# Kernel optimization log

Hardware: AMD Instinct MI355X
Metric: run time of the kernel (lower is better)

The kernel has to match this reference:

```python
import jax, jax.numpy as jnp
import numpy as np

B, S, H, E, I = 2, 2048, 1024, 8, 4096
NUM_SELECT = 2


def setup_inputs() -> dict:
    key = jax.random.key(0)
    ks = jax.random.split(key, 6)
    scale = 0.02
    x = jax.random.normal(ks[0], (B, S, H), dtype=jnp.float32)
    Wg = jax.random.normal(ks[1], (H, E), dtype=jnp.float32) * scale
    W1 = jax.random.normal(ks[2], (E, H, I), dtype=jnp.float32) * scale
    b1 = jnp.zeros((E, I), dtype=jnp.float32)
    W2 = jax.random.normal(ks[3], (E, I, H), dtype=jnp.float32) * scale
    b2 = jnp.zeros((E, H), dtype=jnp.float32)
    return {"x": x, "Wg": Wg, "W1": W1, "b1": b1, "W2": W2, "b2": b2}


def reference(x, Wg, W1, b1, W2, b2):
    b, s, h = x.shape
    e = Wg.shape[1]
    xf = x.reshape(-1, h)                       # [T, H], T = b*s
    T = xf.shape[0]

    logits = xf @ Wg                            # [T, E]
    probs = jax.nn.softmax(logits, axis=-1)
    topk_p, topk_i = jax.lax.top_k(probs, NUM_SELECT)   # [T, k]
    topk_p = topk_p / topk_p.sum(axis=-1, keepdims=True)

    # combine weight per (token, expert): w[t, e] = sum_k topk_p[t, k] * 1[topk_i[t, k] == e]
    # top_k indices within a row are distinct, so scatter-add is exact.
    w = jnp.zeros((T, e), dtype=xf.dtype).at[jnp.arange(T)[:, None], topk_i].add(topk_p)

    # Dense per-expert FFN, weighted combine (weight is 0 for unrouted tokens,
    # so math matches the masked gather/scatter loop of the original).
    out = jnp.zeros_like(xf)
    for ei in range(e):  # small fixed loop over experts
        hdn = jax.nn.silu(xf @ W1[ei] + b1[ei])          # [T, I]
        y = hdn @ W2[ei] + b2[ei]                        # [T, H]
        out = out + w[:, ei:ei + 1] * y
    return out.reshape(b, s, h)
```

## Files before the change

kernel.cpp:

```cpp
#include <hip/hip_runtime.h>
#include <cstdint>
#include <cstddef>

using u16 = unsigned short;
typedef __bf16 bf16x8 __attribute__((ext_vector_type(8)));
typedef float f32x4 __attribute__((ext_vector_type(4)));

#define T_TOK 4096
#define HDIM 1024
#define EXP 8
#define IDIM 4096
#define NROWS 8192
#define PAD_ROWS 8448
#define BM 256
#define MAX_TILES 40

__device__ __forceinline__ u16 f2bf(float f) {
  union { float f; uint32_t u; } v; v.f = f;
  uint32_t u = v.u;
  u += 0x7fffu + ((u >> 16) & 1u);
  return (u16)(u >> 16);
}

__device__ __forceinline__ void async_copy16(const u16* g, u16* s) {
  __builtin_amdgcn_global_load_lds((__attribute__((address_space(1))) void*)(void*)g,
                                   (__attribute__((address_space(3))) void*)s, 16, 0, 0);
}

__global__ __launch_bounds__(256) void gate_kernel(const float* __restrict__ x,
                                                   const float* __restrict__ Wg,
                                                   int* __restrict__ sel_e,
                                                   float* __restrict__ sel_w) {
  int lane = threadIdx.x & 63;
  int wave = threadIdx.x >> 6;
  int t = blockIdx.x * 4 + wave;
  const float* xr = x + (size_t)t * HDIM;
  float p[8];
#pragma unroll
  for (int e = 0; e < 8; ++e) p[e] = 0.f;
#pragma unroll
  for (int i = 0; i < 16; ++i) {
    int h = i * 64 + lane;
    float xv = xr[h];
    const float4* w4 = (const float4*)(Wg + h * 8);
    float4 a = w4[0], b = w4[1];
    p[0] += xv * a.x; p[1] += xv * a.y; p[2] += xv * a.z; p[3] += xv * a.w;
    p[4] += xv * b.x; p[5] += xv * b.y; p[6] += xv * b.z; p[7] += xv * b.w;
  }
#pragma unroll
  for (int e = 0; e < 8; ++e) {
#pragma unroll
    for (int off = 32; off > 0; off >>= 1) p[e] += __shfl_xor(p[e], off);
  }
  if (lane == 0) {
    int e0 = 0; float m0 = p[0];
#pragma unroll
    for (int e = 1; e < 8; ++e) { if (p[e] > m0) { m0 = p[e]; e0 = e; } }
    int e1 = -1; float m1 = -3.4e38f;
#pragma unroll
    for (int e = 0; e < 8; ++e) { if (e != e0 && p[e] > m1) { m1 = p[e]; e1 = e; } }
    float r = expf(m1 - m0);
    float w0 = 1.f / (1.f + r);
    float w1 = r / (1.f + r);
    sel_e[2 * t] = e0; sel_e[2 * t + 1] = e1;
    sel_w[2 * t] = w0; sel_w[2 * t + 1] = w1;
  }
}

__global__ void route_kernel(const int* __restrict__ sel_e, const float* __restrict__ sel_w,
                             int* __restrict__ row_token, float* __restrict__ row_weight,
                             int* __restrict__ tile_m0, int* __restrict__ tile_nrows,
                             int* __restrict__ tile_start, int* __restrict__ tile_cnt,
                             int* __restrict__ work_ctr) {
  __shared__ int cnt[EXP], off[EXP], cur[EXP];
  int tid = threadIdx.x;
  if (tid < EXP) { cnt[tid] = 0; cur[tid] = 0; }
  if (tid < 16) work_ctr[tid] = 0;
  __syncthreads();
  for (int i = tid; i < NROWS; i += 256) atomicAdd(&cnt[sel_e[i]], 1);
  __syncthreads();
  if (tid == 0) {
    int running = 0, nt = 0;
    for (int e = 0; e < EXP; ++e) {
      off[e] = running;
      int c = cnt[e];
      int ntile = (c + BM - 1) / BM;
      tile_start[e] = nt;
      tile_cnt[e] = ntile;
      for (int j = 0; j < ntile; ++j) {
        tile_m0[nt] = running + j * BM;
        tile_nrows[nt] = min(BM, c - j * BM);
        ++nt;
      }
      running += c;
    }
  }
  __syncthreads();
  for (int i = tid; i < NROWS; i += 256) {
    int e = sel_e[i];
    int pos = off[e] + atomicAdd(&cur[e], 1);
    row_token[pos] = i >> 1;
    row_weight[pos] = sel_w[i];
  }
}

__global__ __launch_bounds__(256) void gather_kernel(const float* __restrict__ x,
                                                     const int* __restrict__ row_token,
                                                     u16* __restrict__ xg) {
  int r = blockIdx.x;
  int tok = row_token[r];
  const float4* xs = (const float4*)(x + (size_t)tok * HDIM);
  float4 v = xs[threadIdx.x];
  ushort4 o;
  o.x = f2bf(v.x); o.y = f2bf(v.y); o.z = f2bf(v.z); o.w = f2bf(v.w);
  *(ushort4*)(xg + (size_t)r * HDIM + threadIdx.x * 4) = o;
}

__global__ __launch_bounds__(256) void transpose_convert(const float* __restrict__ src,
                                                         u16* __restrict__ dst, int R, int C) {
  int eb = blockIdx.z;
  const float* s = src + (size_t)eb * R * C;
  u16* d = dst + (size_t)eb * R * C;
  int cb = blockIdx.x * 64, rb = blockIdx.y * 64;
  __shared__ u16 tile[64][65];
  int tid = threadIdx.x;
#pragma unroll
  for (int i = 0; i < 4; ++i) {
    int idx = i * 256 + tid;
    int r = idx >> 4;
    int cq = (idx & 15) * 4;
    float4 v = *(const float4*)(s + (size_t)(rb + r) * C + cb + cq);
    tile[r][cq]     = f2bf(v.x);
    tile[r][cq + 1] = f2bf(v.y);
    tile[r][cq + 2] = f2bf(v.z);
    tile[r][cq + 3] = f2bf(v.w);
  }
  __syncthreads();
#pragma unroll
  for (int i = 0; i < 4; ++i) {
    int idx = i * 256 + tid;
    int c = idx >> 4;
    int rq = (idx & 15) * 4;
    ushort4 o;
    o.x = tile[rq][c]; o.y = tile[rq + 1][c]; o.z = tile[rq + 2][c]; o.w = tile[rq + 3][c];
    *(ushort4*)(d + (size_t)(cb + c) * R + rb + rq) = o;
  }
}

template <int K, int KS, int NB, bool SECOND>
__global__ __launch_bounds__(512, 2) void ffn_gemm8(
    const u16* __restrict__ A, const u16* __restrict__ B,
    const float* __restrict__ bias, u16* __restrict__ hdn_out,
    float* __restrict__ out, const int* __restrict__ row_token,
    const float* __restrict__ row_weight, const int* __restrict__ tile_m0,
    const int* __restrict__ tile_nrows, const int* __restrict__ tile_start,
    const int* __restrict__ tile_cnt, int* __restrict__ ctr, int N) {
  constexpr int KT = K / KS / 64;

  __shared__ u16 sA[2][2 * 128 * 64];
  __shared__ u16 sB[2][128 * 64];
  __shared__ int s_item;

  int tid = threadIdx.x;
  int lane = tid & 63;
  int wave = tid >> 6;
  int wm = wave >> 2, wn = wave & 3;
  int l15 = lane & 15, quad = lane >> 4;
  int r7 = l15 & 7;
  int xcd = blockIdx.x & 7;

  int c0 = tid, c1 = tid + 512;
  int r0s = c0 >> 3, j0 = ((c0 & 7) ^ (r0s & 7)) * 8;
  int r1s = c1 >> 3, j1 = ((c1 & 7) ^ (r1s & 7)) * 8;

  int jxk[2];
#pragma unroll
  for (int ks = 0; ks < 2; ++ks) jxk[ks] = ((ks * 4 + quad) ^ r7) * 8;

  for (int pass = 0; pass < 8; ++pass) {
    int ex = (xcd + pass) & 7;
    int nt_e = tile_cnt[ex];
    if (nt_e == 0) continue;
    int items = nt_e * NB * KS;
    int ts = tile_start[ex];

    for (;;) {
      if (tid == 0) s_item = atomicAdd(&ctr[ex], 1);
      __syncthreads();
      int its = s_item;
      if (its >= items) break;

      int per = NB * nt_e;
      int ksp = its / per;
      int rem = its - ksp * per;
      int nb = rem / nt_e;
      int tile = ts + (rem - nb * nt_e);

      int row0 = tile_m0[tile];
      int nrows = tile_nrows[tile];
      int n0 = nb * 128;
      int korg = ksp * (K / KS);

      const u16* Ab = A + (size_t)row0 * K + korg;
      const u16* Bb = B + (size_t)ex * (size_t)N * K + (size_t)n0 * K + korg;

      auto stageA = [&](int db, int sk, int ha) {
        async_copy16(Ab + (size_t)(ha * 128 + r0s) * K + sk * 64 + j0,
                     &sA[db][ha * 8192 + c0 * 8]);
        async_copy16(Ab + (size_t)(ha * 128 + r1s) * K + sk * 64 + j1,
                     &sA[db][ha * 8192 + c1 * 8]);
      };
      auto stageB = [&](int db, int sk) {
        async_copy16(Bb + (size_t)r0s * K + sk * 64 + j0, &sB[db][c0 * 8]);
        async_copy16(Bb + (size_t)r1s * K + sk * 64 + j1, &sB[db][c1 * 8]);
      };

      f32x4 acc[8][2];
#pragma unroll
      for (int am = 0; am < 8; ++am)
#pragma unroll
        for (int an = 0; an < 2; ++an) acc[am][an] = (f32x4){0.f, 0.f, 0.f, 0.f};

      stageA(0, 0, 0); stageA(0, 0, 1);
      stageB(0, 0);
      stageB(1, 1);
      asm volatile("s_waitcnt vmcnt(2)" ::: "memory");
      __builtin_amdgcn_s_barrier();

      for (int kt = 0; kt < KT; ++kt) {
        int cb = kt & 1, pb = cb ^ 1;
        int ka = kt + 1 < KT ? kt + 1 : KT - 1;
        int kb = kt + 2 < KT ? kt + 2 : KT - 1;
        const u16* sAc = sA[cb];
        const u16* sBc = sB[cb];

        bf16x8 bfr[2][2];
#pragma unroll
        for (int ks = 0; ks < 2; ++ks)
#pragma unroll
          for (int an = 0; an < 2; ++an)
            bfr[an][ks] = *(const bf16x8*)(sBc + ((wn * 2 + an) * 16 + l15) * 64 + jxk[ks]);

        {
          bf16x8 af[4][2];
#pragma unroll
          for (int ks = 0; ks < 2; ++ks)
#pragma unroll
            for (int i = 0; i < 4; ++i)
              af[i][ks] = *(const bf16x8*)(sAc + (wm * 128 + i * 16 + l15) * 64 + jxk[ks]);
          stageA(pb, ka, 0);
          stageA(pb, ka, 1);
          __builtin_amdgcn_s_barrier();
          __builtin_amdgcn_s_setprio(1);
#pragma unroll
          for (int i = 0; i < 4; ++i)
#pragma unroll
            for (int an = 0; an < 2; ++an)
#pragma unroll
              for (int ks = 0; ks < 2; ++ks)
                acc[i][an] = __builtin_amdgcn_mfma_f32_16x16x32_bf16(af[i][ks], bfr[an][ks],
                                                                    acc[i][an], 0, 0, 0);
          __builtin_amdgcn_s_setprio(0);
          __builtin_amdgcn_s_barrier();
        }
        {
          bf16x8 af[4][2];
#pragma unroll
          for (int ks = 0; ks < 2; ++ks)
#pragma unroll
            for (int i = 0; i < 4; ++i)
              af[i][ks] = *(const bf16x8*)(sAc + (wm * 128 + (4 + i) * 16 + l15) * 64 + jxk[ks]);
          stageB(cb, kb);
          asm volatile("s_waitcnt vmcnt(2)" ::: "memory");
          __builtin_amdgcn_s_barrier();
          __builtin_amdgcn_s_setprio(1);
#pragma unroll
          for (int i = 0; i < 4; ++i)
#pragma unroll
            for (int an = 0; an < 2; ++an)
#pragma unroll
              for (int ks = 0; ks < 2; ++ks)
                acc[4 + i][an] = __builtin_amdgcn_mfma_f32_16x16x32_bf16(af[i][ks], bfr[an][ks],
                                                                        acc[4 + i][an], 0, 0, 0);
          __builtin_amdgcn_s_setprio(0);
          __builtin_amdgcn_s_barrier();
        }
      }
      asm volatile("s_waitcnt vmcnt(0)" ::: "memory");

      if constexpr (!SECOND) {
#pragma unroll
        for (int an = 0; an < 2; ++an) {
          int col = n0 + (wn * 2 + an) * 16 + l15;
          float bv = bias[ex * N + col];
#pragma unroll
          for (int am = 0; am < 8; ++am) {
#pragma unroll
            for (int r = 0; r < 4; ++r) {
              int lr = wm * 128 + am * 16 + quad * 4 + r;
              if (lr < nrows) {
                float vv = acc[am][an][r] + bv;
                vv = vv / (1.f + __expf(-vv));
                hdn_out[(size_t)(row0 + lr) * N + col] = f2bf(vv);
              }
            }
          }
        }
      } else {
        float bv[2];
#pragma unroll
        for (int an = 0; an < 2; ++an)
          bv[an] = (ksp == 0) ? bias[ex * N + n0 + (wn * 2 + an) * 16 + l15] : 0.f;
#pragma unroll
        for (int am = 0; am < 8; ++am) {
#pragma unroll
          for (int r = 0; r < 4; ++r) {
            int lr = wm * 128 + am * 16 + quad * 4 + r;
            if (lr < nrows) {
              int grow = row0 + lr;
              int tok = row_token[grow];
              float w = row_weight[grow];
              float* orow = out + (size_t)tok * N;
#pragma unroll
              for (int an = 0; an < 2; ++an) {
                int col = n0 + (wn * 2 + an) * 16 + l15;
                atomicAdd(orow + col, (acc[am][an][r] + bv[an]) * w);
              }
            }
          }
        }
      }
    }
  }
}

extern "C" void kernel_launch(void* const* d_in, const int* in_sizes, int n_in,
                              void* d_out, int out_size, void* d_ws, size_t ws_size,
                              hipStream_t stream) {
  const float* x  = (const float*)d_in[0];
  const float* Wg = (const float*)d_in[1];
  const float* W1 = (const float*)d_in[2];
  const float* b1 = (const float*)d_in[3];
  const float* W2 = (const float*)d_in[4];
  const float* b2 = (const float*)d_in[5];
  float* out = (float*)d_out;

  char* ws = (char*)d_ws;
  size_t off = 0;
  auto alloc = [&](size_t bytes) {
    void* p = ws + off;
    off += (bytes + 255) & ~(size_t)255;
    return p;
  };
  u16* W1T = (u16*)alloc((size_t)EXP * IDIM * HDIM * 2);
  u16* W2T = (u16*)alloc((size_t)EXP * IDIM * HDIM * 2);
  u16* xg  = (u16*)alloc((size_t)PAD_ROWS * HDIM * 2);
  u16* hdn = (u16*)alloc((size_t)PAD_ROWS * IDIM * 2);
  int*   sel_e      = (int*)alloc(NROWS * 4);
  float* sel_w      = (float*)alloc(NROWS * 4);
  int*   row_token  = (int*)alloc(NROWS * 4);
  float* row_weight = (float*)alloc(NROWS * 4);
  int* tile_m0    = (int*)alloc(MAX_TILES * 4);
  int* tile_nrows = (int*)alloc(MAX_TILES * 4);
  int* tile_start = (int*)alloc(EXP * 4);
  int* tile_cnt   = (int*)alloc(EXP * 4);
  int* work_ctr   = (int*)alloc(16 * 4);

  hipMemsetAsync(d_out, 0, (size_t)out_size * sizeof(float), stream);
  transpose_convert<<<dim3(IDIM / 64, HDIM / 64, EXP), 256, 0, stream>>>(W1, W1T, HDIM, IDIM);
  transpose_convert<<<dim3(HDIM / 64, IDIM / 64, EXP), 256, 0, stream>>>(W2, W2T, IDIM, HDIM);
  gate_kernel<<<T_TOK / 4, 256, 0, stream>>>(x, Wg, sel_e, sel_w);
  route_kernel<<<1, 256, 0, stream>>>(sel_e, sel_w, row_token, row_weight,
                                      tile_m0, tile_nrows, tile_start, tile_cnt, work_ctr);
  gather_kernel<<<NROWS, 256, 0, stream>>>(x, row_token, xg);
  ffn_gemm8<HDIM, 1, 32, false><<<256, 512, 0, stream>>>(
      xg, W1T, b1, hdn, nullptr, nullptr, nullptr,
      tile_m0, tile_nrows, tile_start, tile_cnt, work_ctr + 0, IDIM);
  ffn_gemm8<IDIM, 2, 8, true><<<256, 512, 0, stream>>>(
      hdn, W2T, b2, nullptr, out, row_token, row_weight,
      tile_m0, tile_nrows, tile_start, tile_cnt, work_ctr + 8, HDIM);
}
```

Measured before the change: 682.5 us.

## Widen GEMM tile N to 256 and split pipeline into four MFMA phases

Doubles the output tile width from 128 to 256 columns, so each wave computes an 8x4 block of 16x16 MFMA tiles and each A tile loaded into shared memory is reused across twice as many columns. The k-loop now runs in four phases, each loading two A fragments and interleaving one async stage copy (two A halves, two B halves) with the MFMAs. The second GEMM's K split rises from 2 to 4 so there are still enough work items. The cost is more accumulator registers under launch_bounds(512,2), larger shared memory (64KB per block), and more atomic partial-sum traffic in the second GEMM.

Result: slower. 739.2 us (+8.3%).

```diff
diff --git a/kernel.cpp b/kernel.cpp
--- a/kernel.cpp
+++ b/kernel.cpp
@@ -157,8 +157,8 @@
     const int* __restrict__ tile_cnt, int* __restrict__ ctr, int N) {
   constexpr int KT = K / KS / 64;
 
-  __shared__ u16 sA[2][2 * 128 * 64];
-  __shared__ u16 sB[2][128 * 64];
+  __shared__ u16 sA[2][2 * 8192];
+  __shared__ u16 sB[2][2 * 8192];
   __shared__ int s_item;
 
   int tid = threadIdx.x;
@@ -177,6 +177,16 @@
 #pragma unroll
   for (int ks = 0; ks < 2; ++ks) jxk[ks] = ((ks * 4 + quad) ^ r7) * 8;
 
+  int aoff[8];
+#pragma unroll
+  for (int rr = 0; rr < 8; ++rr) aoff[rr] = wm * 8192 + (rr * 16 + l15) * 64;
+  int boff[4];
+#pragma unroll
+  for (int an = 0; an < 4; ++an) {
+    int w = wn * 4 + an;
+    boff[an] = (w >> 3) * 8192 + ((w & 7) * 16 + l15) * 64;
+  }
+
   for (int pass = 0; pass < 8; ++pass) {
     int ex = (xcd + pass) & 7;
     int nt_e = tile_cnt[ex];
@@ -198,7 +208,7 @@
 
       int row0 = tile_m0[tile];
       int nrows = tile_nrows[tile];
-      int n0 = nb * 128;
+      int n0 = nb * 256;
       int korg = ksp * (K / KS);
 
       const u16* Ab = A + (size_t)row0 * K + korg;
@@ -210,88 +220,102 @@
         async_copy16(Ab + (size_t)(ha * 128 + r1s) * K + sk * 64 + j1,
                      &sA[db][ha * 8192 + c1 * 8]);
       };
-      auto stageB = [&](int db, int sk) {
-        async_copy16(Bb + (size_t)r0s * K + sk * 64 + j0, &sB[db][c0 * 8]);
-        async_copy16(Bb + (size_t)r1s * K + sk * 64 + j1, &sB[db][c1 * 8]);
+      auto stageB = [&](int db, int sk, int hb) {
+        async_copy16(Bb + (size_t)(hb * 128 + r0s) * K + sk * 64 + j0,
+                     &sB[db][hb * 8192 + c0 * 8]);
+        async_copy16(Bb + (size_t)(hb * 128 + r1s) * K + sk * 64 + j1,
+                     &sB[db][hb * 8192 + c1 * 8]);
       };
 
-      f32x4 acc[8][2];
+      f32x4 acc[8][4];
 #pragma unroll
       for (int am = 0; am < 8; ++am)
 #pragma unroll
-        for (int an = 0; an < 2; ++an) acc[am][an] = (f32x4){0.f, 0.f, 0.f, 0.f};
+        for (int an = 0; an < 4; ++an) acc[am][an] = (f32x4){0.f, 0.f, 0.f, 0.f};
 
       stageA(0, 0, 0); stageA(0, 0, 1);
-      stageB(0, 0);
-      stageB(1, 1);
-      asm volatile("s_waitcnt vmcnt(2)" ::: "memory");
+      stageB(0, 0, 0); stageB(0, 0, 1);
+      stageB(1, 1, 0); stageB(1, 1, 1);
+      asm volatile("s_waitcnt vmcnt(4)" ::: "memory");
       __builtin_amdgcn_s_barrier();
 
+#define MFMA_PAIR(Q)                                                          \
+      __builtin_amdgcn_s_barrier();                                           \
+      __builtin_amdgcn_s_setprio(1);                                          \
+      _Pragma("unroll")                                                       \
+      for (int i = 0; i < 2; ++i)                                             \
+        _Pragma("unroll")                                                     \
+        for (int an = 0; an < 4; ++an)                                        \
+          _Pragma("unroll")                                                   \
+          for (int ks = 0; ks < 2; ++ks)                                      \
+            acc[2 * (Q) + i][an] = __builtin_amdgcn_mfma_f32_16x16x32_bf16(   \
+                af[i][ks], bfr[an][ks], acc[2 * (Q) + i][an], 0, 0, 0);       \
+      __builtin_amdgcn_s_setprio(0);                                          \
+      __builtin_amdgcn_s_barrier();
+
       for (int kt = 0; kt < KT; ++kt) {
-        int cb = kt & 1, pb = cb ^ 1;
+        int cur = kt & 1, nxt = cur ^ 1;
         int ka = kt + 1 < KT ? kt + 1 : KT - 1;
         int kb = kt + 2 < KT ? kt + 2 : KT - 1;
-        const u16* sAc = sA[cb];
-        const u16* sBc = sB[cb];
-
-        bf16x8 bfr[2][2];
+        const u16* sAc = sA[cur];
+        const u16* sBc = sB[cur];
+
+        bf16x8 bfr[4][2];
 #pragma unroll
         for (int ks = 0; ks < 2; ++ks)
 #pragma unroll
-          for (int an = 0; an < 2; ++an)
-            bfr[an][ks] = *(const bf16x8*)(sBc + ((wn * 2 + an) * 16 + l15) * 64 + jxk[ks]);
+          for (int an = 0; an < 4; ++an)
+            bfr[an][ks] = *(const bf16x8*)(sBc + boff[an] + jxk[ks]);
 
         {
-          bf16x8 af[4][2];
+          bf16x8 af[2][2];
 #pragma unroll
           for (int ks = 0; ks < 2; ++ks)
 #pragma unroll
-            for (int i = 0; i < 4; ++i)
-              af[i][ks] = *(const bf16x8*)(sAc + (wm * 128 + i * 16 + l15) * 64 + jxk[ks]);
-          stageA(pb, ka, 0);
-          stageA(pb, ka, 1);
-          __builtin_amdgcn_s_barrier();
-          __builtin_amdgcn_s_setprio(1);
-#pragma unroll
-          for (int i = 0; i < 4; ++i)
-#pragma unroll
-            for (int an = 0; an < 2; ++an)
-#pragma unroll
-              for (int ks = 0; ks < 2; ++ks)
-                acc[i][an] = __builtin_amdgcn_mfma_f32_16x16x32_bf16(af[i][ks], bfr[an][ks],
-                                                                    acc[i][an], 0, 0, 0);
-          __builtin_amdgcn_s_setprio(0);
-          __builtin_amdgcn_s_barrier();
+            for (int i = 0; i < 2; ++i)
+              af[i][ks] = *(const bf16x8*)(sAc + aoff[i] + jxk[ks]);
+          stageA(nxt, ka, 0);
+          MFMA_PAIR(0)
         }
         {
-          bf16x8 af[4][2];
+          bf16x8 af[2][2];
 #pragma unroll
           for (int ks = 0; ks < 2; ++ks)
 #pragma unroll
-            for (int i = 0; i < 4; ++i)
-              af[i][ks] = *(const bf16x8*)(sAc + (wm * 128 + (4 + i) * 16 + l15) * 64 + jxk[ks]);
-          stageB(cb, kb);
-          asm volatile("s_waitcnt vmcnt(2)" ::: "memory");
-          __builtin_amdgcn_s_barrier();
-          __builtin_amdgcn_s_setprio(1);
-#pragma unroll
-          for (int i = 0; i < 4; ++i)
-#pragma unroll
-            for (int an = 0; an < 2; ++an)
-#pragma unroll
-              for (int ks = 0; ks < 2; ++ks)
-                acc[4 + i][an] = __builtin_amdgcn_mfma_f32_16x16x32_bf16(af[i][ks], bfr[an][ks],
-                                                                        acc[4 + i][an], 0, 0, 0);
-          __builtin_amdgcn_s_setprio(0);
-          __builtin_amdgcn_s_barrier();
+            for (int i = 0; i < 2; ++i)
+              af[i][ks] = *(const bf16x8*)(sAc + aoff[2 + i] + jxk[ks]);
+          stageA(nxt, ka, 1);
+          MFMA_PAIR(1)
+        }
+        {
+          bf16x8 af[2][2];
+#pragma unroll
+          for (int ks = 0; ks < 2; ++ks)
+#pragma unroll
+            for (int i = 0; i < 2; ++i)
+              af[i][ks] = *(const bf16x8*)(sAc + aoff[4 + i] + jxk[ks]);
+          stageB(cur, kb, 0);
+          MFMA_PAIR(2)
+        }
+        {
+          bf16x8 af[2][2];
+#pragma unroll
+          for (int ks = 0; ks < 2; ++ks)
+#pragma unroll
+            for (int i = 0; i < 2; ++i)
+              af[i][ks] = *(const bf16x8*)(sAc + aoff[6 + i] + jxk[ks]);
+          stageB(cur, kb, 1);
+          asm volatile("s_waitcnt vmcnt(4)" ::: "memory");
+          MFMA_PAIR(3)
         }
       }
+#undef MFMA_PAIR
       asm volatile("s_waitcnt vmcnt(0)" ::: "memory");
 
       if constexpr (!SECOND) {
 #pragma unroll
-        for (int an = 0; an < 2; ++an) {
-          int col = n0 + (wn * 2 + an) * 16 + l15;
+        for (int an = 0; an < 4; ++an) {
+          int col = n0 + (wn * 4 + an) * 16 + l15;
           float bv = bias[ex * N + col];
 #pragma unroll
           for (int am = 0; am < 8; ++am) {
@@ -307,10 +331,10 @@
           }
         }
       } else {
-        float bv[2];
-#pragma unroll
-        for (int an = 0; an < 2; ++an)
-          bv[an] = (ksp == 0) ? bias[ex * N + n0 + (wn * 2 + an) * 16 + l15] : 0.f;
+        float bv[4];
+#pragma unroll
+        for (int an = 0; an < 4; ++an)
+          bv[an] = (ksp == 0) ? bias[ex * N + n0 + (wn * 4 + an) * 16 + l15] : 0.f;
 #pragma unroll
         for (int am = 0; am < 8; ++am) {
 #pragma unroll
@@ -322,8 +346,8 @@
               float w = row_weight[grow];
               float* orow = out + (size_t)tok * N;
 #pragma unroll
-              for (int an = 0; an < 2; ++an) {
-                int col = n0 + (wn * 2 + an) * 16 + l15;
+              for (int an = 0; an < 4; ++an) {
+                int col = n0 + (wn * 4 + an) * 16 + l15;
                 atomicAdd(orow + col, (acc[am][an][r] + bv[an]) * w);
               }
             }
@@ -373,10 +397,10 @@
   route_kernel<<<1, 256, 0, stream>>>(sel_e, sel_w, row_token, row_weight,
                                       tile_m0, tile_nrows, tile_start, tile_cnt, work_ctr);
   gather_kernel<<<NROWS, 256, 0, stream>>>(x, row_token, xg);
-  ffn_gemm8<HDIM, 1, 32, false><<<256, 512, 0, stream>>>(
+  ffn_gemm8<HDIM, 1, 16, false><<<256, 512, 0, stream>>>(
       xg, W1T, b1, hdn, nullptr, nullptr, nullptr,
       tile_m0, tile_nrows, tile_start, tile_cnt, work_ctr + 0, IDIM);
-  ffn_gemm8<IDIM, 2, 8, true><<<256, 512, 0, stream>>>(
+  ffn_gemm8<IDIM, 4, 4, true><<<256, 512, 0, stream>>>(
       hdn, W2T, b2, nullptr, out, row_token, row_weight,
       tile_m0, tile_nrows, tile_start, tile_cnt, work_ctr + 8, HDIM);
 }
```
